# Kernel optimization log

Hardware: AMD Instinct MI355X
Metric: run time of the kernel (lower is better)

The kernel has to match this reference:

```python
import jax, jax.numpy as jnp
import numpy as np

B, H, W, C = 64, 14, 14, 768

def setup_inputs() -> dict:
    key = jax.random.key(0)
    k = jax.random.split(key, 5)
    s = 0.02  # small init so tanh/sigmoid stay in active range
    return {
        "x": jax.random.normal(k[0], (B, H, W, C), dtype=jnp.float32),
        "Wx": jax.random.normal(k[1], (3 * C, C), dtype=jnp.float32) * s,
        "bx": jnp.zeros((3 * C,), dtype=jnp.float32),
        "Wh": jax.random.normal(k[2], (3 * C, C), dtype=jnp.float32) * s,
        "bh": jnp.zeros((3 * C,), dtype=jnp.float32),
        "Wp": jax.random.normal(k[3], (C, C), dtype=jnp.float32) * s,
    }

def reference(x, Wx, bx, Wh, bh, Wp):
    b, h_, w_, c = x.shape
    n = h_ * w_
    seq = x.reshape(b, n, c)
    # Input projections for all timesteps at once (no recurrent dependency).
    x_zrn = jnp.einsum('bnc,dc->bnd', seq, Wx) + bx  # [B, N, 3C]
    x_zrn_t = jnp.transpose(x_zrn, (1, 0, 2))        # [N, B, 3C] for scan

    def step(h, xz):
        h_zrn = h @ Wh.T + bh                         # [B, 3C]
        x_z, x_r, x_n = jnp.split(xz, 3, axis=-1)
        h_z, h_r, h_n = jnp.split(h_zrn, 3, axis=-1)
        z = jax.nn.sigmoid(x_z + h_z)
        r = jax.nn.sigmoid(x_r + h_r)
        ncand = jnp.tanh(x_n + r * h_n)
        h_new = (1.0 - z) * ncand + z * h
        return h_new, h_new

    h0 = jnp.zeros((b, c), dtype=x.dtype)
    _, hs = jax.lax.scan(step, h0, x_zrn_t)           # hs: [N, B, C]
    y = jnp.transpose(hs, (1, 0, 2))                  # [B, N, C]
    y = jnp.einsum('bnc,dc->bnd', y, Wp)              # proj (no bias)
    # proj_drop = 0.0 -> identity
    return y.reshape(b, h_, w_, c)
```

## Files before the change

### kernel.cpp

```cpp
#include <hip/hip_runtime.h>

typedef unsigned short u16;
typedef unsigned int   u32;
typedef unsigned long long u64;
typedef __attribute__((ext_vector_type(8))) short bf16x8;
typedef __attribute__((ext_vector_type(4))) float f32x4;

#define GK 768
#define NSTEP 196
#define HSTEP 49152
#define PWG 24
#define NGRP 8
#define FLINE 32
#define GUARD (1 << 18)

__device__ __forceinline__ u16 f2bf(float f) {
    u32 u = __float_as_uint(f);
    u = (u + 0x7fffu + ((u >> 16) & 1u)) >> 16;
    return (u16)u;
}
__device__ __forceinline__ float bf2f(u16 h) { return __uint_as_float(((u32)h) << 16); }

__device__ __forceinline__ int agent_load(const int* p) {
    return __hip_atomic_load(p, __ATOMIC_RELAXED, __HIP_MEMORY_SCOPE_AGENT);
}
__device__ __forceinline__ void agent_store(int* p, int v) {
    __hip_atomic_store(p, v, __ATOMIC_RELAXED, __HIP_MEMORY_SCOPE_AGENT);
}

__global__ __launch_bounds__(256) void cvt_kernel(
    const float4* __restrict__ x, const float4* __restrict__ wx,
    const float4* __restrict__ wp,
    u32* __restrict__ xb, u32* __restrict__ wxb, u32* __restrict__ wpb,
    int* __restrict__ flags)
{
    const int N1 = 9633792 / 4, N2 = 1769472 / 4;
    int i = blockIdx.x * 256 + threadIdx.x;
    if (blockIdx.x == 0) flags[threadIdx.x] = 0;
    const float4* src; u32* dst; int off;
    if (i < N1)            { src = x;  dst = xb;  off = i; }
    else if (i < N1 + N2)  { src = wx; dst = wxb; off = i - N1; }
    else                   { src = wp; dst = wpb; off = i - N1 - N2; }
    float4 v = src[off];
    u32 lo = (u32)f2bf(v.x) | ((u32)f2bf(v.y) << 16);
    u32 hi = (u32)f2bf(v.z) | ((u32)f2bf(v.w) << 16);
    dst[(size_t)off * 2]     = lo;
    dst[(size_t)off * 2 + 1] = hi;
}

template<int MODE>
__global__ __launch_bounds__(256) void gemm_bt(
    const u16* __restrict__ A, const u16* __restrict__ B,
    const float* __restrict__ bias, void* __restrict__ outv)
{
    __shared__ u16 As[128 * 40];
    __shared__ u16 Bs[128 * 40];
    const int tid  = threadIdx.x;
    const int lane = tid & 63;
    const int wv   = tid >> 6;
    const int m0 = blockIdx.y * 128;
    const int n0 = blockIdx.x * 128;
    const int wm = (wv & 1) * 64;
    const int wn = (wv >> 1) * 64;

    f32x4 acc[4][4];
#pragma unroll
    for (int i = 0; i < 4; ++i)
#pragma unroll
        for (int j = 0; j < 4; ++j) acc[i][j] = (f32x4){0.f, 0.f, 0.f, 0.f};

    const int r0 = tid >> 2, q0 = tid & 3;
    const u16* gA0 = A + (size_t)(m0 + r0)      * GK + q0 * 8;
    const u16* gA1 = A + (size_t)(m0 + r0 + 64) * GK + q0 * 8;
    const u16* gB0 = B + (size_t)(n0 + r0)      * GK + q0 * 8;
    const u16* gB1 = B + (size_t)(n0 + r0 + 64) * GK + q0 * 8;
    u16* sA0 = As + r0 * 40 + q0 * 8;
    u16* sA1 = As + (r0 + 64) * 40 + q0 * 8;
    u16* sB0 = Bs + r0 * 40 + q0 * 8;
    u16* sB1 = Bs + (r0 + 64) * 40 + q0 * 8;

    const int fr = lane & 15, fq = lane >> 4;
    const u16* fA = As + (wm + fr) * 40 + fq * 8;
    const u16* fB = Bs + (wn + fr) * 40 + fq * 8;

    for (int kt = 0; kt < GK / 32; ++kt) {
        uint4 a0 = *(const uint4*)(gA0 + kt * 32);
        uint4 a1 = *(const uint4*)(gA1 + kt * 32);
        uint4 b0 = *(const uint4*)(gB0 + kt * 32);
        uint4 b1 = *(const uint4*)(gB1 + kt * 32);
        __syncthreads();
        *(uint4*)sA0 = a0; *(uint4*)sA1 = a1;
        *(uint4*)sB0 = b0; *(uint4*)sB1 = b1;
        __syncthreads();
        bf16x8 af[4], bfr[4];
#pragma unroll
        for (int mi = 0; mi < 4; ++mi) af[mi]  = *(const bf16x8*)(fA + mi * 16 * 40);
#pragma unroll
        for (int ni = 0; ni < 4; ++ni) bfr[ni] = *(const bf16x8*)(fB + ni * 16 * 40);
#pragma unroll
        for (int mi = 0; mi < 4; ++mi)
#pragma unroll
            for (int ni = 0; ni < 4; ++ni)
                acc[mi][ni] = __builtin_amdgcn_mfma_f32_16x16x32_bf16(
                    af[mi], bfr[ni], acc[mi][ni], 0, 0, 0);
    }

    if (MODE == 1) {
        u16* out = (u16*)outv;
#pragma unroll
        for (int mi = 0; mi < 4; ++mi) {
#pragma unroll
            for (int ni = 0; ni < 4; ++ni) {
                int col = n0 + wn + ni * 16 + fr;
                float bv = bias[col];
#pragma unroll
                for (int r = 0; r < 4; ++r) {
                    int m = m0 + wm + mi * 16 + fq * 4 + r;
                    int b = m / 196;
                    int nn = m - b * 196;
                    u16 hv = f2bf(acc[mi][ni][r] + bv);
                    int other = __shfl_xor((int)hv, 1, 64);
                    if (!(lane & 1)) {
                        u32 packed = (u32)hv | (((u32)(u16)other) << 16);
                        size_t eidx = ((size_t)nn * 64 + (size_t)b) * 2304 + (size_t)col;
                        *((u32*)out + (eidx >> 1)) = packed;
                    }
                }
            }
        }
    } else {
        float* out = (float*)outv;
#pragma unroll
        for (int mi = 0; mi < 4; ++mi) {
#pragma unroll
            for (int ni = 0; ni < 4; ++ni) {
                int col = n0 + wn + ni * 16 + fr;
#pragma unroll
                for (int r = 0; r < 4; ++r) {
                    int m = m0 + wm + mi * 16 + fq * 4 + r;
                    int b = m & 63;
                    int nn = m >> 6;
                    out[((size_t)b * 196 + nn) * 768 + col] = acc[mi][ni][r];
                }
            }
        }
    }
}

__global__ __launch_bounds__(384) void recur3_kernel(
    const u16* __restrict__ xz, const float* __restrict__ Wh,
    const float* __restrict__ bh, u16* __restrict__ hsx, int* flags)
{
    __shared__ float hzs[2 * 8 * 96];
    const int tid  = threadIdx.x;
    const int bid  = blockIdx.x;
    const int g    = bid / PWG;
    const int s    = bid - g * PWG;
    const int lane = tid & 63;
    const int wv   = tid >> 6;
    const int kh   = wv & 1;
    const int np   = wv >> 1;
    const int fr   = lane & 15, fq = lane >> 4;
    const int c0   = s * 32;
    const int B0   = g * 8;

    __builtin_amdgcn_fence(__ATOMIC_ACQUIRE, "agent");

    bf16x8 bfrag[2][12];
#pragma unroll
    for (int j = 0; j < 2; ++j) {
        int row = np * 768 + c0 + j * 16 + fr;
        const float* wp = Wh + (size_t)row * 768 + kh * 384 + fq * 8;
#pragma unroll
        for (int kk = 0; kk < 12; ++kk) {
            float4 f0 = *(const float4*)(wp + kk * 32);
            float4 f1 = *(const float4*)(wp + kk * 32 + 4);
            bf16x8 b;
            b[0] = (short)f2bf(f0.x); b[1] = (short)f2bf(f0.y);
            b[2] = (short)f2bf(f0.z); b[3] = (short)f2bf(f0.w);
            b[4] = (short)f2bf(f1.x); b[5] = (short)f2bf(f1.y);
            b[6] = (short)f2bf(f1.z); b[7] = (short)f2bf(f1.w);
            bfrag[j][kk] = b;
        }
    }

    const int gb = tid >> 5, gi = tid & 31;
    const int gc = c0 + gi;
    float bh0 = 0.f, bh1 = 0.f, bh2 = 0.f, hold = 0.f;
    if (tid < 256) { bh0 = bh[gc]; bh1 = bh[768 + gc]; bh2 = bh[1536 + gc]; }

    const int pl = lane % PWG;
    int* const myflag      = &flags[g * FLINE + s];
    const int* const pollp = &flags[g * FLINE + pl];

    float xgn0 = 0.f, xgn1 = 0.f, xgn2 = 0.f;
    if (tid < 256) {
        size_t xoff = (size_t)(B0 + gb) * 2304 + gc;
        xgn0 = bf2f(xz[xoff]);
        xgn1 = bf2f(xz[xoff + 768]);
        xgn2 = bf2f(xz[xoff + 1536]);
    }

    for (int n = 0; n < NSTEP; ++n) {
        const float xg0 = xgn0, xg1 = xgn1, xg2 = xgn2;

        f32x4 acc0 = (f32x4){0.f, 0.f, 0.f, 0.f};
        f32x4 acc1 = (f32x4){0.f, 0.f, 0.f, 0.f};

        if (n > 0) {
            if (tid >= 320) {
                int guard = 0;
                for (;;) {
                    int v = agent_load(pollp);
                    if (__all(v >= n)) break;
                    if (++guard > GUARD) break;
                    __builtin_amdgcn_s_sleep(1);
                }
            }
            __syncthreads();

            const u16* ap = hsx + (size_t)(n - 1) * HSTEP
                                + (size_t)(B0 + fr) * 768 + kh * 384 + fq * 8;
            const bool arow = fr < 8;
#pragma unroll
            for (int kk = 0; kk < 12; ++kk) {
                bf16x8 a = arow ? *(const bf16x8*)(ap + kk * 32)
                                : (bf16x8){0, 0, 0, 0, 0, 0, 0, 0};
                acc0 = __builtin_amdgcn_mfma_f32_16x16x32_bf16(a, bfrag[0][kk], acc0, 0, 0, 0);
                acc1 = __builtin_amdgcn_mfma_f32_16x16x32_bf16(a, bfrag[1][kk], acc1, 0, 0, 0);
            }
        }

#pragma unroll
        for (int r = 0; r < 4; ++r) {
            int b = fq * 4 + r;
            if (b < 8) {
                hzs[(kh * 8 + b) * 96 + np * 32 + fr]      = acc0[r];
                hzs[(kh * 8 + b) * 96 + np * 32 + 16 + fr] = acc1[r];
            }
        }
        __syncthreads();

        if (tid < 256) {
            float h0 = hzs[gb * 96 + gi]      + hzs[(8 + gb) * 96 + gi]      + bh0;
            float h1 = hzs[gb * 96 + 32 + gi] + hzs[(8 + gb) * 96 + 32 + gi] + bh1;
            float h2 = hzs[gb * 96 + 64 + gi] + hzs[(8 + gb) * 96 + 64 + gi] + bh2;
            float z   = 1.f / (1.f + __expf(-(xg0 + h0)));
            float rr2 = 1.f / (1.f + __expf(-(xg1 + h1)));
            float pre = xg2 + rr2 * h2;
            float e2  = __expf(-2.f * pre);
            float nc  = (1.f - e2) / (1.f + e2);
            float hnew = (1.f - z) * nc + z * hold;
            hold = hnew;

            u16 hv = f2bf(hnew);
            u32 other = ((u32)__shfl_xor((int)hv, 1, 64)) & 0xffffu;
            u32 v01 = (u32)hv | (other << 16);
            u32 v23 = (u32)__shfl_xor((int)v01, 2, 64);
            if ((tid & 3) == 0) {
                u64 q = (u64)v01 | ((u64)v23 << 32);
                size_t ofs = (size_t)n * HSTEP + (size_t)(B0 + gb) * 768 + gc;
                __hip_atomic_store((u64*)(hsx + ofs), q,
                                   __ATOMIC_RELAXED, __HIP_MEMORY_SCOPE_AGENT);
            }
        }
        asm volatile("s_waitcnt vmcnt(0)" ::: "memory");
        __syncthreads();
        if (tid == 0) agent_store(myflag, n + 1);

        if (tid < 256) {
            int np1 = (n + 1 < NSTEP) ? n + 1 : NSTEP - 1;
            size_t xoff = ((size_t)np1 * 64 + (B0 + gb)) * 2304 + gc;
            xgn0 = bf2f(xz[xoff]);
            xgn1 = bf2f(xz[xoff + 768]);
            xgn2 = bf2f(xz[xoff + 1536]);
        }
    }
}

extern "C" void kernel_launch(void* const* d_in, const int* in_sizes, int n_in,
                              void* d_out, int out_size, void* d_ws, size_t ws_size,
                              hipStream_t stream)
{
    const float* x  = (const float*)d_in[0];
    const float* Wx = (const float*)d_in[1];
    const float* bx = (const float*)d_in[2];
    const float* Wh = (const float*)d_in[3];
    const float* bh = (const float*)d_in[4];
    const float* Wp = (const float*)d_in[5];
    float* out = (float*)d_out;

    char* ws = (char*)d_ws;
    size_t off = 0;
    auto wsalloc = [&](size_t bytes) -> void* {
        void* p = ws + off;
        off += (bytes + 255) & ~(size_t)255;
        return p;
    };
    u16* xb   = (u16*)wsalloc(9633792ull * 2);
    u16* wxb  = (u16*)wsalloc(1769472ull * 2);
    u16* wpb  = (u16*)wsalloc(589824ull * 2);
    u16* xzrn = (u16*)wsalloc(196ull * 64 * 2304 * 2);
    u16* hsx  = (u16*)wsalloc(196ull * 64 * 768 * 2);
    int* flags = (int*)wsalloc(1024);

    cvt_kernel<<<11712, 256, 0, stream>>>(
        (const float4*)x, (const float4*)Wx, (const float4*)Wp,
        (u32*)xb, (u32*)wxb, (u32*)wpb, flags);

    gemm_bt<1><<<dim3(18, 98), 256, 0, stream>>>(xb, wxb, bx, (void*)xzrn);

    {
        const u16* a0 = xzrn; const float* a1 = Wh; const float* a2 = bh;
        u16* a3 = hsx; int* a4 = flags;
        void* args[5] = { &a0, &a1, &a2, &a3, &a4 };
        hipLaunchCooperativeKernel((void*)recur3_kernel, dim3(NGRP * PWG),
                                   dim3(384), args, 0, stream);
    }

    gemm_bt<0><<<dim3(6, 98), 256, 0, stream>>>(hsx, wpb, nullptr, (void*)out);
}
```

Measured before the change: 1.096 ms.

## Group recurrence workgroups by XCD and poll flags via L2 atomics

Launches 256 cooperative workgroups, and each one reads its XCC id and takes a slot in a per-XCD counter. Each batch group of 24 workgroups is then placed on a single XCD, and surplus workgroups exit. Within the group, per-step flags and h stores go through the XCD-local L2, and consumers poll with atomic-add-zero reads instead of agent-scope loads. The aim is lower cross-XCD synchronisation latency on every one of the 196 serial steps. This relies on undocumented L2 coherence behaviour, and it keeps a mirrored agent-scope flag and h store as a fallback, which adds extra stores and a startup barrier.

Measured after the change: 1.174 ms. 1.07x slower.

```diff
diff --git a/kernel.cpp b/kernel.cpp
--- a/kernel.cpp
+++ b/kernel.cpp
@@ -11,7 +11,10 @@
 #define HSTEP 49152
 #define PWG 24
 #define NGRP 8
+#define NBLK 256
 #define FLINE 32
+#define FLAG0 64
+#define MIR0 6656
 #define GUARD (1 << 18)
 
 __device__ __forceinline__ u16 f2bf(float f) {
@@ -26,6 +29,13 @@
 }
 __device__ __forceinline__ void agent_store(int* p, int v) {
     __hip_atomic_store(p, v, __ATOMIC_RELAXED, __HIP_MEMORY_SCOPE_AGENT);
+}
+__device__ __forceinline__ int atomic_read_l2(int* p) {
+    int v; int zero = 0;
+    asm volatile("global_atomic_add %0, %1, %2, off sc0\n\t"
+                 "s_waitcnt vmcnt(0)"
+                 : "=&v"(v) : "v"(p), "v"(zero) : "memory");
+    return v;
 }
 
 __global__ __launch_bounds__(256) void cvt_kernel(
@@ -36,7 +46,7 @@
 {
     const int N1 = 9633792 / 4, N2 = 1769472 / 4;
     int i = blockIdx.x * 256 + threadIdx.x;
-    if (blockIdx.x == 0) flags[threadIdx.x] = 0;
+    if (blockIdx.x < 32) flags[blockIdx.x * 256 + threadIdx.x] = 0;
     const float4* src; u32* dst; int off;
     if (i < N1)            { src = x;  dst = xb;  off = i; }
     else if (i < N1 + N2)  { src = wx; dst = wxb; off = i - N1; }
@@ -147,15 +157,13 @@
     }
 }
 
-__global__ __launch_bounds__(384) void recur3_kernel(
+template<bool FAST>
+__device__ void recur_core(
+    int g, int s, int tid,
     const u16* __restrict__ xz, const float* __restrict__ Wh,
-    const float* __restrict__ bh, u16* __restrict__ hsx, int* flags)
-{
-    __shared__ float hzs[2 * 8 * 96];
-    const int tid  = threadIdx.x;
-    const int bid  = blockIdx.x;
-    const int g    = bid / PWG;
-    const int s    = bid - g * PWG;
+    const float* __restrict__ bh, u16* __restrict__ hsx, int* flags,
+    float* hzs)
+{
     const int lane = tid & 63;
     const int wv   = tid >> 6;
     const int kh   = wv & 1;
@@ -163,8 +171,6 @@
     const int fr   = lane & 15, fq = lane >> 4;
     const int c0   = s * 32;
     const int B0   = g * 8;
-
-    __builtin_amdgcn_fence(__ATOMIC_ACQUIRE, "agent");
 
     bf16x8 bfrag[2][12];
 #pragma unroll
@@ -190,8 +196,10 @@
     if (tid < 256) { bh0 = bh[gc]; bh1 = bh[768 + gc]; bh2 = bh[1536 + gc]; }
 
     const int pl = lane % PWG;
-    int* const myflag      = &flags[g * FLINE + s];
-    const int* const pollp = &flags[g * FLINE + pl];
+    int* const myflag = &flags[FLAG0 + (g * PWG + s)  * FLINE];
+    int* const pollp  = &flags[FLAG0 + (g * PWG + pl) * FLINE];
+    int* const mymir  = &flags[MIR0 + g * FLINE + s];
+    const int* const pollm = &flags[MIR0 + g * FLINE + pl];
 
     float xgn0 = 0.f, xgn1 = 0.f, xgn2 = 0.f;
     if (tid < 256) {
@@ -201,6 +209,8 @@
         xgn2 = bf2f(xz[xoff + 1536]);
     }
 
+    bool slow = !FAST;
+
     for (int n = 0; n < NSTEP; ++n) {
         const float xg0 = xgn0, xg1 = xgn1, xg2 = xgn2;
 
@@ -209,12 +219,24 @@
 
         if (n > 0) {
             if (tid >= 320) {
-                int guard = 0;
-                for (;;) {
-                    int v = agent_load(pollp);
-                    if (__all(v >= n)) break;
-                    if (++guard > GUARD) break;
-                    __builtin_amdgcn_s_sleep(1);
+                bool done = false;
+                if (FAST && !slow) {
+                    int tries = 0;
+                    for (;;) {
+                        int v = atomic_read_l2(pollp);
+                        if (__all(v >= n)) { done = true; break; }
+                        if (++tries > 4096) { slow = true; break; }
+                        __builtin_amdgcn_s_sleep(1);
+                    }
+                }
+                if (!done) {
+                    int guard = 0;
+                    for (;;) {
+                        int v = agent_load(pollm);
+                        if (__all(v >= n)) break;
+                        if (++guard > GUARD) break;
+                        __builtin_amdgcn_s_sleep(1);
+                    }
                 }
             }
             __syncthreads();
@@ -260,13 +282,16 @@
             if ((tid & 3) == 0) {
                 u64 q = (u64)v01 | ((u64)v23 << 32);
                 size_t ofs = (size_t)n * HSTEP + (size_t)(B0 + gb) * 768 + gc;
-                __hip_atomic_store((u64*)(hsx + ofs), q,
-                                   __ATOMIC_RELAXED, __HIP_MEMORY_SCOPE_AGENT);
+                u64* p = (u64*)(hsx + ofs);
+                *p = q;
+                __hip_atomic_store(p, q, __ATOMIC_RELAXED,
+                                   __HIP_MEMORY_SCOPE_AGENT);
             }
         }
         asm volatile("s_waitcnt vmcnt(0)" ::: "memory");
         __syncthreads();
-        if (tid == 0) agent_store(myflag, n + 1);
+        if (tid == 0)       *myflag = n + 1;
+        else if (tid == 64) agent_store(mymir, n + 1);
 
         if (tid < 256) {
             int np1 = (n + 1 < NSTEP) ? n + 1 : NSTEP - 1;
@@ -275,6 +300,57 @@
             xgn1 = bf2f(xz[xoff + 768]);
             xgn2 = bf2f(xz[xoff + 1536]);
         }
+    }
+}
+
+__global__ __launch_bounds__(384) void recur4_kernel(
+    const u16* __restrict__ xz, const float* __restrict__ Wh,
+    const float* __restrict__ bh, u16* __restrict__ hsx, int* flags)
+{
+    __shared__ float hzs[2 * 8 * 96];
+    __shared__ int sh_mode, sh_g, sh_s;
+    const int tid = threadIdx.x;
+
+    __builtin_amdgcn_fence(__ATOMIC_ACQUIRE, "agent");
+
+    if (tid == 0) {
+        u32 xcc = 0;
+        asm volatile("s_getreg_b32 %0, hwreg(HW_REG_XCC_ID)" : "=s"(xcc));
+        const int my_xcd = (int)(xcc & 7u);
+        const int slot = __hip_atomic_fetch_add(&flags[my_xcd], 1, __ATOMIC_ACQ_REL,
+                                                __HIP_MEMORY_SCOPE_AGENT);
+        __hip_atomic_fetch_add(&flags[15], 1, __ATOMIC_ACQ_REL,
+                               __HIP_MEMORY_SCOPE_AGENT);
+        int guard = 0;
+        while (__hip_atomic_load(&flags[15], __ATOMIC_ACQUIRE,
+                                 __HIP_MEMORY_SCOPE_AGENT) < NBLK) {
+            if (++guard > GUARD) break;
+            __builtin_amdgcn_s_sleep(1);
+        }
+        int G = 0, pre = 0, myg = 0;
+        for (int x = 0; x < 8; ++x) {
+            int c  = agent_load(&flags[x]);
+            int gx = c / PWG;
+            if (x < my_xcd) pre += gx;
+            if (x == my_xcd) myg = gx;
+            G += gx;
+        }
+        const int grp = pre + slot / PWG;
+        const bool act = (slot < myg * PWG) && (grp < NGRP);
+        sh_mode = (G >= NGRP) ? (act ? 1 : 2) : 0;
+        sh_g = grp;
+        sh_s = slot % PWG;
+    }
+    __syncthreads();
+    const int mode = sh_mode;
+
+    if (mode == 1) {
+        recur_core<true>(sh_g, sh_s, tid, xz, Wh, bh, hsx, flags, hzs);
+    } else if (mode == 0) {
+        const int bid = blockIdx.x;
+        if (bid < NGRP * PWG)
+            recur_core<false>(bid / PWG, bid % PWG, tid, xz, Wh, bh, hsx,
+                              flags, hzs);
     }
 }
 
@@ -302,7 +378,7 @@
     u16* wpb  = (u16*)wsalloc(589824ull * 2);
     u16* xzrn = (u16*)wsalloc(196ull * 64 * 2304 * 2);
     u16* hsx  = (u16*)wsalloc(196ull * 64 * 768 * 2);
-    int* flags = (int*)wsalloc(1024);
+    int* flags = (int*)wsalloc(32768);
 
     cvt_kernel<<<11712, 256, 0, stream>>>(
         (const float4*)x, (const float4*)Wx, (const float4*)Wp,
@@ -314,8 +390,8 @@
         const u16* a0 = xzrn; const float* a1 = Wh; const float* a2 = bh;
         u16* a3 = hsx; int* a4 = flags;
         void* args[5] = { &a0, &a1, &a2, &a3, &a4 };
-        hipLaunchCooperativeKernel((void*)recur3_kernel, dim3(NGRP * PWG),
-                                   dim3(384), args, 0, stream);
+        hipLaunchCooperativeKernel((void*)recur4_kernel, dim3(NBLK), dim3(384),
+                                   args, 0, stream);
     }
 
     gemm_bt<0><<<dim3(6, 98), 256, 0, stream>>>(hsx, wpb, nullptr, (void*)out);
```
